# Kernel tuning notes

Measured on AMD Instinct MI355X. Metric: run time of the kernel, lower is better.

The kernel has to match this reference:

```python
import jax, jax.numpy as jnp
import numpy as np

N = 50000    # nodes
E = 800000   # edges (avg degree 16)
IN = 256     # in_dim
HID = 256    # hidden_dim
OUT = 128    # out_dim


def setup_inputs() -> dict:
    key = jax.random.key(0)
    ks = jax.random.split(key, 9)
    features = jax.random.normal(ks[0], (N, IN), jnp.float32)
    src = jax.random.randint(ks[1], (E,), 0, N, jnp.int32)
    dst = jax.random.randint(ks[2], (E,), 0, N, jnp.int32)
    noise = jax.random.normal(ks[3], (N, OUT), jnp.float32)
    def glorot(k, shape, fan):
        return jax.random.normal(k, shape, jnp.float32) / np.float32(np.sqrt(fan))
    W1 = glorot(ks[4], (IN, HID), IN);  b1 = jnp.zeros((HID,), jnp.float32)
    W2 = glorot(ks[5], (HID, OUT), HID); b2 = jnp.zeros((OUT,), jnp.float32)
    W3 = glorot(ks[6], (HID, OUT), HID); b3 = jnp.zeros((OUT,), jnp.float32)
    fcW = glorot(ks[7], (HID, IN), IN)   # nn.Linear(in_dim, hidden_dim).weight: [HID, IN]
    return dict(features=features, noise=noise, W1=W1, b1=b1, W2=W2, b2=b2,
                W3=W3, b3=b3, fcW=fcW, src=src, dst=dst)


def _gcn(x, W, b, src, dst, out_norm, in_norm):
    """DGL GraphConv norm='both': D_out^{-1/2} A D_in^{-1/2} X W + b."""
    x = x * out_norm[:, None]          # scale src features by out-deg^{-1/2}
    x = x @ W                          # dense transform (order commutes with SpMM)
    agg = jax.ops.segment_sum(x[src], dst, num_segments=N)  # sparse aggregate
    return agg * in_norm[:, None] + b


def reference(features, noise, W1, b1, W2, b2, W3, b3, fcW, src, dst):
    ones = jnp.ones((E,), jnp.float32)
    out_deg = jax.ops.segment_sum(ones, src, num_segments=N)
    in_deg = jax.ops.segment_sum(ones, dst, num_segments=N)
    out_norm = jnp.maximum(out_deg, 1.0) ** -0.5
    in_norm = jnp.maximum(in_deg, 1.0) ** -0.5

    h = jax.nn.relu(_gcn(features, W1, b1, src, dst, out_norm, in_norm))
    mean = jax.nn.relu(_gcn(h, W2, b2, src, dst, out_norm, in_norm))
    log_std = _gcn(h, W3, b3, src, dst, out_norm, in_norm)  # identity activation
    z = mean + noise * jnp.exp(log_std)
    seq_fts = features @ fcW.T
    return z, h, seq_fts
```

## Files before the change

### kernel.cpp

```cpp
#include <hip/hip_runtime.h>
#include <hip/hip_bf16.h>
#include <stdint.h>
#include <math.h>

#define IN_DIM 256
#define HID_DIM 256
#define OUT_DIM 128

typedef __attribute__((ext_vector_type(8))) short short8;
typedef __attribute__((ext_vector_type(4))) float floatx4;

__device__ __forceinline__ float bf2f(ushort u) {
  union { uint32_t i; float f; } v; v.i = ((uint32_t)u) << 16; return v.f;
}
__device__ __forceinline__ ushort f2bf(float f) {
  union { float f; uint32_t u; } v; v.f = f;
  uint32_t u = v.u;
  uint32_t r = u + 0x7fffu + ((u >> 16) & 1u);
  return (ushort)(r >> 16);
}

__global__ void deg_prep_kernel(const int* __restrict__ src, const int* __restrict__ dst,
                                int* __restrict__ out_deg, int* __restrict__ in_deg,
                                int E, int eblocks,
                                const float* __restrict__ W1, const float* __restrict__ W2,
                                const float* __restrict__ W3, const float* __restrict__ b2,
                                const float* __restrict__ b3, const float* __restrict__ fcW,
                                ushort* __restrict__ W1T, ushort* __restrict__ WcT,
                                float* __restrict__ bcat, ushort* __restrict__ fcWb) {
  int b = blockIdx.x, t = threadIdx.x;
  if (b < eblocks) {
    int e = (b * 256 + t) * 2;
    if (e + 1 < E) {
      int2 s = *(const int2*)(src + e);
      int2 d = *(const int2*)(dst + e);
      atomicAdd(&out_deg[s.x], 1);
      atomicAdd(&out_deg[s.y], 1);
      atomicAdd(&in_deg[d.x], 1);
      atomicAdd(&in_deg[d.y], 1);
    } else if (e < E) {
      atomicAdd(&out_deg[src[e]], 1);
      atomicAdd(&in_deg[dst[e]], 1);
    }
  } else if (b < eblocks + 256) {
    int k = b - eblocks;
    int nn = t;
    W1T[nn * 256 + k] = f2bf(W1[k * 256 + nn]);
    WcT[nn * 256 + k] = f2bf((nn < 128) ? W2[k * 128 + nn] : W3[k * 128 + (nn - 128)]);
    if (k == 0) bcat[nn] = (nn < 128) ? b2[nn] : b3[nn - 128];
  } else {
    int k = b - eblocks - 256;
    fcWb[k * 256 + t] = f2bf(fcW[k * 256 + t]);
  }
}

__global__ __launch_bounds__(256, 2) void mega_kernel(
    const float* __restrict__ feat, const ushort* __restrict__ fcWb,
    const ushort* __restrict__ W1T,
    float* __restrict__ s_out, ushort* __restrict__ xw1_bf,
    const int* __restrict__ in_deg, int* __restrict__ row_ptr, int n, int M, int gb) {
  __shared__ alignas(16) ushort A_lds[128 * 64];
  __shared__ alignas(16) ushort B_lds[256 * 64];
  int b = blockIdx.x;
  int t = threadIdx.x;

  if (b == 0) {
    int* lds = (int*)A_lds;
    int CH = (n + 255) >> 8; CH = (CH + 3) & ~3;
    int base = t * CH;
    int s = 0;
    if (base + CH <= n) {
      const int4* p = (const int4*)(in_deg + base);
      int c4 = CH >> 2;
#pragma unroll 8
      for (int j = 0; j < c4; ++j) { int4 q = p[j]; s += q.x + q.y + q.z + q.w; }
    } else {
      for (int i = base; i < n; ++i) s += in_deg[i];
    }
    lds[t] = s;
    __syncthreads();
    for (int off = 1; off < 256; off <<= 1) {
      int add = (t >= off) ? lds[t - off] : 0;
      __syncthreads();
      lds[t] += add;
      __syncthreads();
    }
    int run = lds[t] - s;
    if (t == 0) row_ptr[0] = 0;
    if (base + CH <= n) {
      const int4* p = (const int4*)(in_deg + base);
      int c4 = CH >> 2;
#pragma unroll 4
      for (int j = 0; j < c4; ++j) {
        int4 q = p[j];
        int i = base + j * 4;
        run += q.x; row_ptr[i + 1] = run;
        run += q.y; row_ptr[i + 2] = run;
        run += q.z; row_ptr[i + 3] = run;
        run += q.w; row_ptr[i + 4] = run;
      }
    } else {
      for (int i = base; i < n; ++i) { run += in_deg[i]; row_ptr[i + 1] = run; }
    }
    return;
  }

  int bb = b - 1;
  bool isSeq = bb < gb;
  int m0 = (isSeq ? bb : bb - gb) * 128;
  const ushort* Bsrc = isSeq ? fcWb : W1T;
  int wave = t >> 6, lane = t & 63;
  int wm = wave * 32;
  int l15 = lane & 15, quad = lane >> 4;

  floatx4 acc[2][16];
#pragma unroll
  for (int i = 0; i < 2; ++i)
#pragma unroll
    for (int j = 0; j < 16; ++j) acc[i][j] = (floatx4)(0.f);

  for (int kc = 0; kc < 256; kc += 64) {
#pragma unroll
    for (int r = 0; r < 8; ++r) {
      int idx = t + r * 256;
      int row = idx >> 4;
      int c = (idx & 15) << 2;
      int grow = m0 + row; if (grow > M - 1) grow = M - 1;
      float4 v = *(const float4*)(feat + (size_t)grow * 256 + kc + c);
      ushort4 o;
      o.x = f2bf(v.x); o.y = f2bf(v.y); o.z = f2bf(v.z); o.w = f2bf(v.w);
      int sc = c ^ ((row & 7) << 3);
      *(ushort4*)&A_lds[row * 64 + sc] = o;
    }
#pragma unroll
    for (int r = 0; r < 8; ++r) {
      int idx = t + r * 256;
      int row = idx >> 3;
      int c = (idx & 7) << 3;
      int sc = c ^ ((row & 7) << 3);
      *(uint4*)&B_lds[row * 64 + sc] = *(const uint4*)(Bsrc + (size_t)row * 256 + kc + c);
    }
    __syncthreads();
#pragma unroll
    for (int ko = 0; ko < 2; ++ko) {
      short8 a[2];
#pragma unroll
      for (int i = 0; i < 2; ++i) {
        int row = wm + i * 16 + l15;
        int sc = (ko * 32 + quad * 8) ^ ((l15 & 7) << 3);
        a[i] = *(const short8*)&A_lds[row * 64 + sc];
      }
#pragma unroll
      for (int j = 0; j < 16; ++j) {
        int brow = j * 16 + l15;
        int sc = (ko * 32 + quad * 8) ^ ((l15 & 7) << 3);
        short8 bv = *(const short8*)&B_lds[brow * 64 + sc];
#pragma unroll
        for (int i = 0; i < 2; ++i)
          acc[i][j] = __builtin_amdgcn_mfma_f32_16x16x32_bf16(a[i], bv, acc[i][j], 0, 0, 0);
      }
    }
    __syncthreads();
  }

  if (isSeq) {
#pragma unroll
    for (int i = 0; i < 2; ++i)
#pragma unroll
      for (int j = 0; j < 16; ++j) {
        int col = j * 16 + l15;
#pragma unroll
        for (int r = 0; r < 4; ++r) {
          int row = m0 + wm + i * 16 + quad * 4 + r;
          if (row < M) s_out[(size_t)row * 256 + col] = acc[i][j][r];
        }
      }
  } else {
#pragma unroll
    for (int i = 0; i < 2; ++i)
#pragma unroll
      for (int j = 0; j < 16; ++j) {
        int col = j * 16 + l15;
#pragma unroll
        for (int r = 0; r < 4; ++r) {
          int row = m0 + wm + i * 16 + quad * 4 + r;
          if (row < M) xw1_bf[(size_t)row * 256 + col] = f2bf(acc[i][j][r]);
        }
      }
  }
}

__global__ void fill_kernel(const int* __restrict__ src, const int* __restrict__ dst,
                            const int* __restrict__ row_ptr, int* __restrict__ fill_cnt,
                            const int* __restrict__ out_deg,
                            int2* __restrict__ edge_sw, int E) {
  int e = (blockIdx.x * 256 + threadIdx.x) * 2;
  if (e + 1 < E) {
    int2 s = *(const int2*)(src + e);
    int2 d = *(const int2*)(dst + e);
    int pos0 = row_ptr[d.x] + atomicAdd(&fill_cnt[d.x], 1);
    int od0 = out_deg[s.x]; if (od0 < 1) od0 = 1;
    int2 r0; r0.x = s.x; r0.y = __float_as_int(rsqrtf((float)od0));
    edge_sw[pos0] = r0;
    int pos1 = row_ptr[d.y] + atomicAdd(&fill_cnt[d.y], 1);
    int od1 = out_deg[s.y]; if (od1 < 1) od1 = 1;
    int2 r1; r1.x = s.y; r1.y = __float_as_int(rsqrtf((float)od1));
    edge_sw[pos1] = r1;
  } else if (e < E) {
    int d = dst[e]; int s = src[e];
    int pos = row_ptr[d] + atomicAdd(&fill_cnt[d], 1);
    int od = out_deg[s]; if (od < 1) od = 1;
    int2 r; r.x = s; r.y = __float_as_int(rsqrtf((float)od));
    edge_sw[pos] = r;
  }
}

__global__ __launch_bounds__(256) void agg_kernel(
    const ushort* __restrict__ x, const int* __restrict__ row_ptr,
    const int2* __restrict__ edge_sw,
    const float* __restrict__ bias, const float* __restrict__ noise,
    float* __restrict__ out32, ushort* __restrict__ outbf, int N, int mode) {
  int wave = threadIdx.x >> 6, lane = threadIdx.x & 63;
  int n = blockIdx.x * 4 + wave;
  if (n >= N) return;
  int half = lane >> 5;
  int hl = lane & 31;
  int start = row_ptr[n], end = row_ptr[n + 1];
  int dg = end - start; if (dg < 1) dg = 1;
  float inn = rsqrtf((float)dg);

  float acc[8];
#pragma unroll
  for (int k = 0; k < 8; ++k) acc[k] = 0.f;

  for (int base = start; base < end; base += 16) {
    int cs[8]; float cw[8];
    if (base + 16 <= end) {
#pragma unroll
      for (int k = 0; k < 8; ++k) {
        int2 e = edge_sw[base + half + 2 * k];
        cs[k] = e.x; cw[k] = __int_as_float(e.y);
      }
    } else {
#pragma unroll
      for (int k = 0; k < 8; ++k) {
        int i = base + half + 2 * k;
        cs[k] = 0; cw[k] = 0.f;
        if (i < end) { int2 e = edge_sw[i]; cs[k] = e.x; cw[k] = __int_as_float(e.y); }
      }
    }
    uint4 v[8];
#pragma unroll
    for (int k = 0; k < 8; ++k)
      v[k] = *(const uint4*)&x[(size_t)cs[k] * 256 + hl * 8];
#pragma unroll
    for (int k = 0; k < 8; ++k) {
      const uint32_t* p = (const uint32_t*)&v[k];
      float wk = cw[k];
#pragma unroll
      for (int q = 0; q < 4; ++q) {
        acc[2 * q]     += bf2f((ushort)(p[q] & 0xffffu)) * wk;
        acc[2 * q + 1] += bf2f((ushort)(p[q] >> 16)) * wk;
      }
    }
  }

#pragma unroll
  for (int k = 0; k < 8; ++k) acc[k] += __shfl_xor(acc[k], 32, 64);

  if (mode == 0) {
    if (half == 0) {
      int c0 = hl * 8;
      float4 ba = *(const float4*)(bias + c0);
      float4 bb = *(const float4*)(bias + c0 + 4);
      float h[8];
      h[0] = fmaxf(acc[0] * inn + ba.x, 0.f);
      h[1] = fmaxf(acc[1] * inn + ba.y, 0.f);
      h[2] = fmaxf(acc[2] * inn + ba.z, 0.f);
      h[3] = fmaxf(acc[3] * inn + ba.w, 0.f);
      h[4] = fmaxf(acc[4] * inn + bb.x, 0.f);
      h[5] = fmaxf(acc[5] * inn + bb.y, 0.f);
      h[6] = fmaxf(acc[6] * inn + bb.z, 0.f);
      h[7] = fmaxf(acc[7] * inn + bb.w, 0.f);
      *(float4*)&out32[(size_t)n * 256 + c0] = make_float4(h[0], h[1], h[2], h[3]);
      *(float4*)&out32[(size_t)n * 256 + c0 + 4] = make_float4(h[4], h[5], h[6], h[7]);
      uint4 ob; uint32_t* po = (uint32_t*)&ob;
#pragma unroll
      for (int q = 0; q < 4; ++q)
        po[q] = ((uint32_t)f2bf(h[2 * q + 1]) << 16) | (uint32_t)f2bf(h[2 * q]);
      *(uint4*)&outbf[(size_t)n * 256 + c0] = ob;
    }
  } else {
    float pacc[8];
#pragma unroll
    for (int k = 0; k < 8; ++k) pacc[k] = __shfl(acc[k], (lane & 15) + 16, 64);
    if (lane < 16) {
      int c0 = lane * 8;
      float4 b2a = *(const float4*)(bias + c0);
      float4 b2b = *(const float4*)(bias + c0 + 4);
      float4 b3a = *(const float4*)(bias + 128 + c0);
      float4 b3b = *(const float4*)(bias + 128 + c0 + 4);
      float4 nza = *(const float4*)(noise + (size_t)n * 128 + c0);
      float4 nzb = *(const float4*)(noise + (size_t)n * 128 + c0 + 4);
      float z[8];
      z[0] = fmaxf(acc[0] * inn + b2a.x, 0.f) + nza.x * expf(pacc[0] * inn + b3a.x);
      z[1] = fmaxf(acc[1] * inn + b2a.y, 0.f) + nza.y * expf(pacc[1] * inn + b3a.y);
      z[2] = fmaxf(acc[2] * inn + b2a.z, 0.f) + nza.z * expf(pacc[2] * inn + b3a.z);
      z[3] = fmaxf(acc[3] * inn + b2a.w, 0.f) + nza.w * expf(pacc[3] * inn + b3a.w);
      z[4] = fmaxf(acc[4] * inn + b2b.x, 0.f) + nzb.x * expf(pacc[4] * inn + b3b.x);
      z[5] = fmaxf(acc[5] * inn + b2b.y, 0.f) + nzb.y * expf(pacc[5] * inn + b3b.y);
      z[6] = fmaxf(acc[6] * inn + b2b.z, 0.f) + nzb.z * expf(pacc[6] * inn + b3b.z);
      z[7] = fmaxf(acc[7] * inn + b2b.w, 0.f) + nzb.w * expf(pacc[7] * inn + b3b.w);
      *(float4*)&out32[(size_t)n * 128 + c0] = make_float4(z[0], z[1], z[2], z[3]);
      *(float4*)&out32[(size_t)n * 128 + c0 + 4] = make_float4(z[4], z[5], z[6], z[7]);
    }
  }
}

__global__ __launch_bounds__(256, 2) void gemm_bf_kernel(
    const ushort* __restrict__ A, const ushort* __restrict__ BT,
    ushort* __restrict__ Cbf, int M) {
  __shared__ alignas(16) ushort A_lds[128 * 64];
  __shared__ alignas(16) ushort B_lds[256 * 64];
  int t = threadIdx.x;
  int m0 = blockIdx.x * 128;
  int wave = t >> 6, lane = t & 63;
  int wm = wave * 32;
  int l15 = lane & 15, quad = lane >> 4;

  floatx4 acc[2][16];
#pragma unroll
  for (int i = 0; i < 2; ++i)
#pragma unroll
    for (int j = 0; j < 16; ++j) acc[i][j] = (floatx4)(0.f);

  for (int kc = 0; kc < 256; kc += 64) {
#pragma unroll
    for (int r = 0; r < 4; ++r) {
      int idx = t + r * 256;
      int row = idx >> 3;
      int c = (idx & 7) << 3;
      int grow = m0 + row; if (grow > M - 1) grow = M - 1;
      int sc = c ^ ((row & 7) << 3);
      *(uint4*)&A_lds[row * 64 + sc] = *(const uint4*)(A + (size_t)grow * 256 + kc + c);
    }
#pragma unroll
    for (int r = 0; r < 8; ++r) {
      int idx = t + r * 256;
      int row = idx >> 3;
      int c = (idx & 7) << 3;
      int sc = c ^ ((row & 7) << 3);
      *(uint4*)&B_lds[row * 64 + sc] = *(const uint4*)(BT + (size_t)row * 256 + kc + c);
    }
    __syncthreads();
#pragma unroll
    for (int ko = 0; ko < 2; ++ko) {
      short8 a[2];
#pragma unroll
      for (int i = 0; i < 2; ++i) {
        int row = wm + i * 16 + l15;
        int sc = (ko * 32 + quad * 8) ^ ((l15 & 7) << 3);
        a[i] = *(const short8*)&A_lds[row * 64 + sc];
      }
#pragma unroll
      for (int j = 0; j < 16; ++j) {
        int brow = j * 16 + l15;
        int sc = (ko * 32 + quad * 8) ^ ((l15 & 7) << 3);
        short8 bv = *(const short8*)&B_lds[brow * 64 + sc];
#pragma unroll
        for (int i = 0; i < 2; ++i)
          acc[i][j] = __builtin_amdgcn_mfma_f32_16x16x32_bf16(a[i], bv, acc[i][j], 0, 0, 0);
      }
    }
    __syncthreads();
  }

#pragma unroll
  for (int i = 0; i < 2; ++i)
#pragma unroll
    for (int j = 0; j < 16; ++j) {
      int col = j * 16 + l15;
#pragma unroll
      for (int r = 0; r < 4; ++r) {
        int row = m0 + wm + i * 16 + quad * 4 + r;
        if (row < M) Cbf[(size_t)row * 256 + col] = f2bf(acc[i][j][r]);
      }
    }
}

extern "C" void kernel_launch(void* const* d_in, const int* in_sizes, int n_in,
                              void* d_out, int out_size, void* d_ws, size_t ws_size,
                              hipStream_t stream) {
  const float* features = (const float*)d_in[0];
  const float* noise    = (const float*)d_in[1];
  const float* W1 = (const float*)d_in[2];
  const float* b1 = (const float*)d_in[3];
  const float* W2 = (const float*)d_in[4];
  const float* b2 = (const float*)d_in[5];
  const float* W3 = (const float*)d_in[6];
  const float* b3 = (const float*)d_in[7];
  const float* fcW = (const float*)d_in[8];
  const int* src = (const int*)d_in[9];
  const int* dst = (const int*)d_in[10];
  const int N = in_sizes[0] / IN_DIM;
  const int E = in_sizes[9];

  float* out = (float*)d_out;
  float* z_out = out;
  float* h_out = out + (size_t)N * OUT_DIM;
  float* s_out = h_out + (size_t)N * HID_DIM;

  char* w = (char*)d_ws;
  auto carve = [&](size_t bytes) {
    char* p = w;
    w += (bytes + 255) & ~(size_t)255;
    return p;
  };
  ushort* xw1_bf = (ushort*)carve((size_t)N * 256 * 2);
  ushort* h_bf   = (ushort*)carve((size_t)N * 256 * 2);
  ushort* hwc_bf = (ushort*)carve((size_t)N * 256 * 2);
  ushort* W1T  = (ushort*)carve(256 * 256 * 2);
  ushort* WcT  = (ushort*)carve(256 * 256 * 2);
  ushort* fcWb = (ushort*)carve(256 * 256 * 2);
  float*  bcat = (float*)carve(256 * 4);
  int* degs    = (int*)carve((size_t)3 * N * 4);
  int* out_deg = degs;
  int* in_deg  = degs + N;
  int* fill_cnt = degs + 2 * N;
  int* row_ptr  = (int*)carve((size_t)(N + 1) * 4);
  int2* edge_sw = (int2*)carve((size_t)E * 8);

  hipMemsetAsync(degs, 0, (size_t)3 * N * 4, stream);
  int eblocks = ((E + 1) / 2 + 255) / 256;
  int gb = (N + 127) / 128;

  deg_prep_kernel<<<eblocks + 512, 256, 0, stream>>>(src, dst, out_deg, in_deg, E, eblocks,
                                                     W1, W2, W3, b2, b3, fcW,
                                                     W1T, WcT, bcat, fcWb);
  mega_kernel<<<2 * gb + 1, 256, 0, stream>>>(features, fcWb, W1T, s_out, xw1_bf,
                                              in_deg, row_ptr, N, N, gb);
  fill_kernel<<<eblocks, 256, 0, stream>>>(src, dst, row_ptr, fill_cnt, out_deg,
                                           edge_sw, E);
  agg_kernel<<<(N + 3) / 4, 256, 0, stream>>>(xw1_bf, row_ptr, edge_sw, b1,
                                              (const float*)nullptr, h_out, h_bf, N, 0);
  gemm_bf_kernel<<<gb, 256, 0, stream>>>(h_bf, WcT, hwc_bf, N);
  agg_kernel<<<(N + 3) / 4, 256, 0, stream>>>(hwc_bf, row_ptr, edge_sw, bcat,
                                              noise, z_out, (ushort*)nullptr, N, 1);
}
```

Before: 492.9 us.

## Drop LDS staging in GEMMs; load MFMA fragments directly from pre-packed weights

```diff
diff --git a/kernel.cpp b/kernel.cpp
--- a/kernel.cpp
+++ b/kernel.cpp
@@ -18,6 +18,18 @@
   uint32_t u = v.u;
   uint32_t r = u + 0x7fffu + ((u >> 16) & 1u);
   return (ushort)(r >> 16);
+}
+__device__ __forceinline__ short8 pack_bf16x8(float4 a, float4 b) {
+  short8 r;
+  r[0] = (short)f2bf(a.x); r[1] = (short)f2bf(a.y);
+  r[2] = (short)f2bf(a.z); r[3] = (short)f2bf(a.w);
+  r[4] = (short)f2bf(b.x); r[5] = (short)f2bf(b.y);
+  r[6] = (short)f2bf(b.z); r[7] = (short)f2bf(b.w);
+  return r;
+}
+
+__device__ __forceinline__ int bpack_idx(int n, int k) {
+  return ((k >> 3) * 2048) + ((n & 15) * 128) + ((n >> 4) * 8) + (k & 7);
 }
 
 __global__ void deg_prep_kernel(const int* __restrict__ src, const int* __restrict__ dst,
@@ -26,8 +38,8 @@
                                 const float* __restrict__ W1, const float* __restrict__ W2,
                                 const float* __restrict__ W3, const float* __restrict__ b2,
                                 const float* __restrict__ b3, const float* __restrict__ fcW,
-                                ushort* __restrict__ W1T, ushort* __restrict__ WcT,
-                                float* __restrict__ bcat, ushort* __restrict__ fcWb) {
+                                ushort* __restrict__ W1Tp, ushort* __restrict__ WcTp,
+                                float* __restrict__ bcat, ushort* __restrict__ fcWp) {
   int b = blockIdx.x, t = threadIdx.x;
   if (b < eblocks) {
     int e = (b * 256 + t) * 2;
@@ -45,27 +57,26 @@
   } else if (b < eblocks + 256) {
     int k = b - eblocks;
     int nn = t;
-    W1T[nn * 256 + k] = f2bf(W1[k * 256 + nn]);
-    WcT[nn * 256 + k] = f2bf((nn < 128) ? W2[k * 128 + nn] : W3[k * 128 + (nn - 128)]);
+    W1Tp[bpack_idx(nn, k)] = f2bf(W1[k * 256 + nn]);
+    WcTp[bpack_idx(nn, k)] = f2bf((nn < 128) ? W2[k * 128 + nn] : W3[k * 128 + (nn - 128)]);
     if (k == 0) bcat[nn] = (nn < 128) ? b2[nn] : b3[nn - 128];
   } else {
     int k = b - eblocks - 256;
-    fcWb[k * 256 + t] = f2bf(fcW[k * 256 + t]);
+    int nn = t;
+    fcWp[bpack_idx(k, nn)] = f2bf(fcW[k * 256 + nn]);
   }
 }
 
 __global__ __launch_bounds__(256, 2) void mega_kernel(
-    const float* __restrict__ feat, const ushort* __restrict__ fcWb,
-    const ushort* __restrict__ W1T,
+    const float* __restrict__ feat, const ushort* __restrict__ fcWp,
+    const ushort* __restrict__ W1Tp,
     float* __restrict__ s_out, ushort* __restrict__ xw1_bf,
     const int* __restrict__ in_deg, int* __restrict__ row_ptr, int n, int M, int gb) {
-  __shared__ alignas(16) ushort A_lds[128 * 64];
-  __shared__ alignas(16) ushort B_lds[256 * 64];
+  __shared__ int slds[256];
   int b = blockIdx.x;
   int t = threadIdx.x;
 
   if (b == 0) {
-    int* lds = (int*)A_lds;
     int CH = (n + 255) >> 8; CH = (CH + 3) & ~3;
     int base = t * CH;
     int s = 0;
@@ -77,15 +88,15 @@
     } else {
       for (int i = base; i < n; ++i) s += in_deg[i];
     }
-    lds[t] = s;
+    slds[t] = s;
     __syncthreads();
     for (int off = 1; off < 256; off <<= 1) {
-      int add = (t >= off) ? lds[t - off] : 0;
+      int add = (t >= off) ? slds[t - off] : 0;
       __syncthreads();
-      lds[t] += add;
+      slds[t] += add;
       __syncthreads();
     }
-    int run = lds[t] - s;
+    int run = slds[t] - s;
     if (t == 0) row_ptr[0] = 0;
     if (base + CH <= n) {
       const int4* p = (const int4*)(in_deg + base);
@@ -108,59 +119,37 @@
   int bb = b - 1;
   bool isSeq = bb < gb;
   int m0 = (isSeq ? bb : bb - gb) * 128;
-  const ushort* Bsrc = isSeq ? fcWb : W1T;
+  const ushort* Bp = isSeq ? fcWp : W1Tp;
   int wave = t >> 6, lane = t & 63;
   int wm = wave * 32;
   int l15 = lane & 15, quad = lane >> 4;
 
+  int r0 = m0 + wm + l15;      if (r0 > M - 1) r0 = M - 1;
+  int r1 = m0 + wm + 16 + l15; if (r1 > M - 1) r1 = M - 1;
+  const float* pa0 = feat + (size_t)r0 * 256 + quad * 8;
+  const float* pa1 = feat + (size_t)r1 * 256 + quad * 8;
+
   floatx4 acc[2][16];
 #pragma unroll
   for (int i = 0; i < 2; ++i)
 #pragma unroll
     for (int j = 0; j < 16; ++j) acc[i][j] = (floatx4)(0.f);
 
-  for (int kc = 0; kc < 256; kc += 64) {
-#pragma unroll
-    for (int r = 0; r < 8; ++r) {
-      int idx = t + r * 256;
-      int row = idx >> 4;
-      int c = (idx & 15) << 2;
-      int grow = m0 + row; if (grow > M - 1) grow = M - 1;
-      float4 v = *(const float4*)(feat + (size_t)grow * 256 + kc + c);
-      ushort4 o;
-      o.x = f2bf(v.x); o.y = f2bf(v.y); o.z = f2bf(v.z); o.w = f2bf(v.w);
-      int sc = c ^ ((row & 7) << 3);
-      *(ushort4*)&A_lds[row * 64 + sc] = o;
-    }
-#pragma unroll
-    for (int r = 0; r < 8; ++r) {
-      int idx = t + r * 256;
-      int row = idx >> 3;
-      int c = (idx & 7) << 3;
-      int sc = c ^ ((row & 7) << 3);
-      *(uint4*)&B_lds[row * 64 + sc] = *(const uint4*)(Bsrc + (size_t)row * 256 + kc + c);
-    }
-    __syncthreads();
-#pragma unroll
-    for (int ko = 0; ko < 2; ++ko) {
-      short8 a[2];
-#pragma unroll
-      for (int i = 0; i < 2; ++i) {
-        int row = wm + i * 16 + l15;
-        int sc = (ko * 32 + quad * 8) ^ ((l15 & 7) << 3);
-        a[i] = *(const short8*)&A_lds[row * 64 + sc];
-      }
-#pragma unroll
-      for (int j = 0; j < 16; ++j) {
-        int brow = j * 16 + l15;
-        int sc = (ko * 32 + quad * 8) ^ ((l15 & 7) << 3);
-        short8 bv = *(const short8*)&B_lds[brow * 64 + sc];
-#pragma unroll
-        for (int i = 0; i < 2; ++i)
-          acc[i][j] = __builtin_amdgcn_mfma_f32_16x16x32_bf16(a[i], bv, acc[i][j], 0, 0, 0);
-      }
-    }
-    __syncthreads();
+#pragma unroll
+  for (int ks = 0; ks < 8; ++ks) {
+    float4 v0 = *(const float4*)(pa0 + ks * 32);
+    float4 v1 = *(const float4*)(pa0 + ks * 32 + 4);
+    float4 w0 = *(const float4*)(pa1 + ks * 32);
+    float4 w1 = *(const float4*)(pa1 + ks * 32 + 4);
+    short8 a0 = pack_bf16x8(v0, v1);
+    short8 a1 = pack_bf16x8(w0, w1);
+    const ushort* pb = Bp + ((ks * 4 + quad) * 16 + l15) * 128;
+#pragma unroll
+    for (int j = 0; j < 16; ++j) {
+      short8 bv = *(const short8*)(pb + j * 8);
+      acc[0][j] = __builtin_amdgcn_mfma_f32_16x16x32_bf16(a0, bv, acc[0][j], 0, 0, 0);
+      acc[1][j] = __builtin_amdgcn_mfma_f32_16x16x32_bf16(a1, bv, acc[1][j], 0, 0, 0);
+    }
   }
 
   if (isSeq) {
@@ -318,61 +307,36 @@
 }
 
 __global__ __launch_bounds__(256, 2) void gemm_bf_kernel(
-    const ushort* __restrict__ A, const ushort* __restrict__ BT,
+    const ushort* __restrict__ A, const ushort* __restrict__ Bp,
     ushort* __restrict__ Cbf, int M) {
-  __shared__ alignas(16) ushort A_lds[128 * 64];
-  __shared__ alignas(16) ushort B_lds[256 * 64];
   int t = threadIdx.x;
   int m0 = blockIdx.x * 128;
   int wave = t >> 6, lane = t & 63;
   int wm = wave * 32;
   int l15 = lane & 15, quad = lane >> 4;
 
+  int r0 = m0 + wm + l15;      if (r0 > M - 1) r0 = M - 1;
+  int r1 = m0 + wm + 16 + l15; if (r1 > M - 1) r1 = M - 1;
+  const ushort* pa0 = A + (size_t)r0 * 256 + quad * 8;
+  const ushort* pa1 = A + (size_t)r1 * 256 + quad * 8;
+
   floatx4 acc[2][16];
 #pragma unroll
   for (int i = 0; i < 2; ++i)
 #pragma unroll
     for (int j = 0; j < 16; ++j) acc[i][j] = (floatx4)(0.f);
 
-  for (int kc = 0; kc < 256; kc += 64) {
-#pragma unroll
-    for (int r = 0; r < 4; ++r) {
-      int idx = t + r * 256;
-      int row = idx >> 3;
-      int c = (idx & 7) << 3;
-      int grow = m0 + row; if (grow > M - 1) grow = M - 1;
-      int sc = c ^ ((row & 7) << 3);
-      *(uint4*)&A_lds[row * 64 + sc] = *(const uint4*)(A + (size_t)grow * 256 + kc + c);
-    }
-#pragma unroll
-    for (int r = 0; r < 8; ++r) {
-      int idx = t + r * 256;
-      int row = idx >> 3;
-      int c = (idx & 7) << 3;
-      int sc = c ^ ((row & 7) << 3);
-      *(uint4*)&B_lds[row * 64 + sc] = *(const uint4*)(BT + (size_t)row * 256 + kc + c);
-    }
-    __syncthreads();
-#pragma unroll
-    for (int ko = 0; ko < 2; ++ko) {
-      short8 a[2];
-#pragma unroll
-      for (int i = 0; i < 2; ++i) {
-        int row = wm + i * 16 + l15;
-        int sc = (ko * 32 + quad * 8) ^ ((l15 & 7) << 3);
-        a[i] = *(const short8*)&A_lds[row * 64 + sc];
-      }
-#pragma unroll
-      for (int j = 0; j < 16; ++j) {
-        int brow = j * 16 + l15;
-        int sc = (ko * 32 + quad * 8) ^ ((l15 & 7) << 3);
-        short8 bv = *(const short8*)&B_lds[brow * 64 + sc];
-#pragma unroll
-        for (int i = 0; i < 2; ++i)
-          acc[i][j] = __builtin_amdgcn_mfma_f32_16x16x32_bf16(a[i], bv, acc[i][j], 0, 0, 0);
-      }
-    }
-    __syncthreads();
+#pragma unroll
+  for (int ks = 0; ks < 8; ++ks) {
+    short8 a0 = *(const short8*)(pa0 + ks * 32);
+    short8 a1 = *(const short8*)(pa1 + ks * 32);
+    const ushort* pb = Bp + ((ks * 4 + quad) * 16 + l15) * 128;
+#pragma unroll
+    for (int j = 0; j < 16; ++j) {
+      short8 bv = *(const short8*)(pb + j * 8);
+      acc[0][j] = __builtin_amdgcn_mfma_f32_16x16x32_bf16(a0, bv, acc[0][j], 0, 0, 0);
+      acc[1][j] = __builtin_amdgcn_mfma_f32_16x16x32_bf16(a1, bv, acc[1][j], 0, 0, 0);
+    }
   }
 
 #pragma unroll
@@ -419,9 +383,9 @@
   ushort* xw1_bf = (ushort*)carve((size_t)N * 256 * 2);
   ushort* h_bf   = (ushort*)carve((size_t)N * 256 * 2);
   ushort* hwc_bf = (ushort*)carve((size_t)N * 256 * 2);
-  ushort* W1T  = (ushort*)carve(256 * 256 * 2);
-  ushort* WcT  = (ushort*)carve(256 * 256 * 2);
-  ushort* fcWb = (ushort*)carve(256 * 256 * 2);
+  ushort* W1Tp = (ushort*)carve(256 * 256 * 2);
+  ushort* WcTp = (ushort*)carve(256 * 256 * 2);
+  ushort* fcWp = (ushort*)carve(256 * 256 * 2);
   float*  bcat = (float*)carve(256 * 4);
   int* degs    = (int*)carve((size_t)3 * N * 4);
   int* out_deg = degs;
@@ -436,14 +400,14 @@
 
   deg_prep_kernel<<<eblocks + 512, 256, 0, stream>>>(src, dst, out_deg, in_deg, E, eblocks,
                                                      W1, W2, W3, b2, b3, fcW,
-                                                     W1T, WcT, bcat, fcWb);
-  mega_kernel<<<2 * gb + 1, 256, 0, stream>>>(features, fcWb, W1T, s_out, xw1_bf,
+                                                     W1Tp, WcTp, bcat, fcWp);
+  mega_kernel<<<2 * gb + 1, 256, 0, stream>>>(features, fcWp, W1Tp, s_out, xw1_bf,
                                               in_deg, row_ptr, N, N, gb);
   fill_kernel<<<eblocks, 256, 0, stream>>>(src, dst, row_ptr, fill_cnt, out_deg,
                                            edge_sw, E);
   agg_kernel<<<(N + 3) / 4, 256, 0, stream>>>(xw1_bf, row_ptr, edge_sw, b1,
                                               (const float*)nullptr, h_out, h_bf, N, 0);
-  gemm_bf_kernel<<<gb, 256, 0, stream>>>(h_bf, WcT, hwc_bf, N);
+  gemm_bf_kernel<<<gb, 256, 0, stream>>>(h_bf, WcTp, hwc_bf, N);
   agg_kernel<<<(N + 3) / 4, 256, 0, stream>>>(hwc_bf, row_ptr, edge_sw, bcat,
                                               noise, z_out, (ushort*)nullptr, N, 1);
 }
```

After: 535.2 us. +8.6%, slower.
